# Kernel tuning notes

Measured on AMD Instinct MI355X. Metric: run time of the kernel, lower is better.

Reference implementation:

```python
import jax, jax.numpy as jnp
import numpy as np

B, N, E = 2, 32768, 32768
DIM = 3
MP_STEPS = 2
H = 32  # hidden width; original bug: depth == hidden width (range(hidden))


def _ln(x, g, b):
    m = jnp.mean(x, axis=-1, keepdims=True)
    v = jnp.var(x, axis=-1, keepdims=True)
    return (x - m) * jax.lax.rsqrt(v + 1e-5) * g + b


def _mlp(x, Win, bin_, Wh, bh, Wout, bout, lng=None, lnb=None):
    # Linear -> ReLU -> [LN] -> H x (Linear -> ReLU -> [LN]) -> Linear -> ReLU
    h = jax.nn.relu(x @ Win + bin_)
    if lng is not None:
        h = _ln(h, lng[0], lnb[0])
        def body(h, p):
            W, b_, g_, bb = p
            return _ln(jax.nn.relu(h @ W + b_), g_, bb), None
        h, _ = jax.lax.scan(body, h, (Wh, bh, lng[1:], lnb[1:]))
    else:
        def body(h, p):
            W, b_ = p
            return jax.nn.relu(h @ W + b_), None
        h, _ = jax.lax.scan(body, h, (Wh, bh))
    return jax.nn.relu(h @ Wout + bout)


def _mk(key, din, h, dout, ln, pref):
    ks = jax.random.split(key, 3)
    d = {
        pref + 'Win': jax.random.normal(ks[0], (din, h), jnp.float32) / np.sqrt(din).astype(np.float32),
        pref + 'bin': jnp.zeros((h,), jnp.float32),
        pref + 'Wh': jax.random.normal(ks[1], (h, h, h), jnp.float32) / np.sqrt(h).astype(np.float32),
        pref + 'bh': jnp.zeros((h, h), jnp.float32),
        pref + 'Wout': jax.random.normal(ks[2], (h, dout), jnp.float32) / np.sqrt(h).astype(np.float32),
        pref + 'bout': jnp.zeros((dout,), jnp.float32),
    }
    if ln:
        d[pref + 'lng'] = jnp.ones((h + 1, h), jnp.float32)
        d[pref + 'lnb'] = jnp.zeros((h + 1, h), jnp.float32)
    return d


def setup_inputs() -> dict:
    key = jax.random.key(0)
    ks = jax.random.split(key, 10)
    inp = {
        'nodes': jax.random.normal(ks[0], (B, N, 6), jnp.float32),
        'edges': jax.random.normal(ks[1], (B, E, 1), jnp.float32),
        'gvec': jax.random.normal(ks[2], (B,), jnp.float32),
        'senders': jax.random.randint(ks[3], (B, E), 0, N, jnp.int32),
        'receivers': jax.random.randint(ks[4], (B, E), 0, N, jnp.int32),
    }
    inp.update(_mk(ks[5], 6 + 1, H, 16, False, 'ne_'))          # node encoder: node_dim+global
    inp.update(_mk(ks[6], 1 + DIM + 1, H, 16, False, 'ed_'))    # edge encoder: edge_dim+dim+1
    inp.update(_mk(ks[7], 16 + 2 * 16 + 1, H, 16, True, 'pe_')) # edge processor
    inp.update(_mk(ks[8], 16 + 16 + 1, H, 16, True, 'pv_'))     # node processor
    inp.update(_mk(ks[9], 16, H, DIM, False, 'de_'))            # decoder
    return inp


def reference(nodes, edges, gvec, senders, receivers,
              ne_Win, ne_bin, ne_Wh, ne_bh, ne_Wout, ne_bout,
              ed_Win, ed_bin, ed_Wh, ed_bh, ed_Wout, ed_bout,
              pe_Win, pe_bin, pe_Wh, pe_bh, pe_Wout, pe_bout, pe_lng, pe_lnb,
              pv_Win, pv_bin, pv_Wh, pv_bh, pv_Wout, pv_bout, pv_lng, pv_lnb,
              de_Win, de_bin, de_Wh, de_bh, de_Wout, de_bout):
    g_node = jnp.broadcast_to(gvec[:, None, None], (B, N, 1))  # global repeated per node
    g_edge = jnp.broadcast_to(gvec[:, None, None], (B, E, 1))  # global repeated per edge
    x = jnp.concatenate([nodes, g_node], axis=-1)  # [B,N,7]

    # relative edge features from sender/receiver positions (first DIM cols)
    pos = x[..., :DIM]
    si = senders[:, :, None]
    ri = receivers[:, :, None]
    rel = jnp.take_along_axis(pos, si, axis=1) - jnp.take_along_axis(pos, ri, axis=1)  # [B,E,3]
    nrm = jnp.linalg.norm(rel, axis=-1, keepdims=True)
    e_in = jnp.concatenate([edges, rel, nrm], axis=-1)  # [B,E,5]

    ve = _mlp(x, ne_Win, ne_bin, ne_Wh, ne_bh, ne_Wout, ne_bout)       # [B,N,16]
    ee = _mlp(e_in, ed_Win, ed_bin, ed_Wh, ed_bh, ed_Wout, ed_bout)    # [B,E,16]

    seg = jax.vmap(lambda e, r: jax.ops.segment_sum(e, r, num_segments=N))

    for _ in range(MP_STEPS):
        # phi_e: gather sender/receiver node states, concat, edge MLP
        vs = jnp.take_along_axis(ve, si, axis=1)  # [B,E,16]
        vr = jnp.take_along_axis(ve, ri, axis=1)
        ee = _mlp(jnp.concatenate([ee, vs, vr, g_edge], axis=-1),
                  pe_Win, pe_bin, pe_Wh, pe_bh, pe_Wout, pe_bout, pe_lng, pe_lnb)
        # phi_v: scatter-add edge states into receiver nodes, concat, node MLP
        agg = seg(ee, receivers)  # [B,N,16]
        ve = _mlp(jnp.concatenate([agg, ve, g_node], axis=-1),
                  pv_Win, pv_bin, pv_Wh, pv_bh, pv_Wout, pv_bout, pv_lng, pv_lnb)

    return _mlp(ve, de_Win, de_bin, de_Wh, de_bh, de_Wout, de_bout)  # [B,N,3]
```

## Files before the change

### kernel.cpp

```cpp
#include <hip/hip_runtime.h>

#define BB 2
#define NN 32768
#define EN 32768

typedef unsigned int u32;
typedef __attribute__((ext_vector_type(8)))  short bf16x8;
typedef __attribute__((ext_vector_type(2)))  float f32x2;
typedef __attribute__((ext_vector_type(16))) float f32x16;

union U4 { uint4 u; bf16x8 h; };

__device__ __forceinline__ u32 pk2(float lo, float hi) {
    u32 r;
    asm("v_cvt_pk_bf16_f32 %0, %1, %2" : "=v"(r) : "v"(lo), "v"(hi));
    return r;
}

__device__ __forceinline__ float xor32_sum(float x) {
    float y = x;
    asm("v_permlane32_swap_b32 %0, %1" : "+v"(x), "+v"(y));
    return x + y;
}

__device__ __forceinline__ f32x16 MF32(bf16x8 a, bf16x8 b, f32x16 c) {
    return __builtin_amdgcn_mfma_f32_32x32x16_bf16(a, b, c, 0, 0, 0);
}

template<bool LN>
__device__ __forceinline__ void transform32(f32x16 D, bf16x8& B0, bf16x8& B1)
{
    f32x2 p0 = {D[0],D[1]},  p1 = {D[2],D[3]},  p2 = {D[4],D[5]},  p3 = {D[6],D[7]};
    f32x2 p4 = {D[8],D[9]},  p5 = {D[10],D[11]},p6 = {D[12],D[13]},p7 = {D[14],D[15]};
    const f32x2 zz = {0.f, 0.f};
    p0 = __builtin_elementwise_max(p0, zz); p1 = __builtin_elementwise_max(p1, zz);
    p2 = __builtin_elementwise_max(p2, zz); p3 = __builtin_elementwise_max(p3, zz);
    p4 = __builtin_elementwise_max(p4, zz); p5 = __builtin_elementwise_max(p5, zz);
    p6 = __builtin_elementwise_max(p6, zz); p7 = __builtin_elementwise_max(p7, zz);
    if (LN) {
        f32x2 sv = ((p0+p1)+(p2+p3)) + ((p4+p5)+(p6+p7));
        f32x2 ta = __builtin_elementwise_fma(p0,p0,
                   __builtin_elementwise_fma(p1,p1,
                   __builtin_elementwise_fma(p2,p2, p3*p3)));
        f32x2 tb = __builtin_elementwise_fma(p4,p4,
                   __builtin_elementwise_fma(p5,p5,
                   __builtin_elementwise_fma(p6,p6, p7*p7)));
        f32x2 tv = ta + tb;
        float s = xor32_sum(sv.x + sv.y);
        float t = xor32_sum(tv.x + tv.y);
        float mu  = s * (1.f/32.f);
        float var = fmaf(-mu, mu, t * (1.f/32.f));
        float rs  = rsqrtf(var + 1e-5f);
        float nt  = -mu * rs;
        f32x2 rs2 = {rs, rs}, nt2 = {nt, nt};
        p0 = __builtin_elementwise_fma(p0, rs2, nt2);
        p1 = __builtin_elementwise_fma(p1, rs2, nt2);
        p2 = __builtin_elementwise_fma(p2, rs2, nt2);
        p3 = __builtin_elementwise_fma(p3, rs2, nt2);
        p4 = __builtin_elementwise_fma(p4, rs2, nt2);
        p5 = __builtin_elementwise_fma(p5, rs2, nt2);
        p6 = __builtin_elementwise_fma(p6, rs2, nt2);
        p7 = __builtin_elementwise_fma(p7, rs2, nt2);
    }
    U4 c;
    c.u.x = pk2(p0.x,p0.y); c.u.y = pk2(p1.x,p1.y);
    c.u.z = pk2(p2.x,p2.y); c.u.w = pk2(p3.x,p3.y);
    B0 = c.h;
    c.u.x = pk2(p4.x,p4.y); c.u.y = pk2(p5.x,p5.y);
    c.u.z = pk2(p6.x,p6.y); c.u.w = pk2(p7.x,p7.y);
    B1 = c.h;
}

__device__ __forceinline__ f32x16 load_biasC(const float* WB, int base, int h) {
    const float4* p = (const float4*)(WB + base + h*16);
    float4 a = p[0], b = p[1], c = p[2], d = p[3];
    f32x16 C = {a.x,a.y,a.z,a.w, b.x,b.y,b.z,b.w,
                c.x,c.y,c.z,c.w, d.x,d.y,d.z,d.w};
    return C;
}

template<int NT, bool LN>
__device__ __forceinline__ f32x16 mlp32(const bf16x8* bIn,
    const u32* WL, const float* WB, int lane, int h)
{
    constexpr int HB = NT*256;
    constexpr int BO = HB + 16384;
    U4 c;
    f32x16 D = load_biasC(WB, 0, h);
    #pragma unroll
    for (int t = 0; t < NT; ++t) {
        c.u = *(const uint4*)(WL + t*256 + lane*4);
        D = MF32(c.h, bIn[t], D);
    }
    c.u = *(const uint4*)(WL + HB + lane*4);        bf16x8 w0 = c.h;
    c.u = *(const uint4*)(WL + HB + 256 + lane*4);  bf16x8 w1 = c.h;
    c.u = *(const uint4*)(WL + HB + 512 + lane*4);  bf16x8 x0 = c.h;
    c.u = *(const uint4*)(WL + HB + 768 + lane*4);  bf16x8 x1 = c.h;
    f32x16 pb = load_biasC(WB, 32, h);
    bf16x8 B0, B1;
    transform32<LN>(D, B0, B1);
    #pragma unroll 4
    for (int l = 0; l < 32; ++l) {
        const int lp = (l+2 < 32) ? l+2 : 31;
        c.u = *(const uint4*)(WL + HB + lp*512 + lane*4);       bf16x8 nw0 = c.h;
        c.u = *(const uint4*)(WL + HB + lp*512 + 256 + lane*4); bf16x8 nw1 = c.h;
        const int lb_ = (l+1 < 32) ? l+1 : 31;
        f32x16 nb = load_biasC(WB, 32 + lb_*32, h);
        f32x16 E = MF32(w0, B0, pb);
        E = MF32(w1, B1, E);
        transform32<LN>(E, B0, B1);
        w0 = x0; w1 = x1; x0 = nw0; x1 = nw1; pb = nb;
    }
    c.u = *(const uint4*)(WL + BO + lane*4);        bf16x8 o0 = c.h;
    c.u = *(const uint4*)(WL + BO + 256 + lane*4);  bf16x8 o1 = c.h;
    f32x16 Co = load_biasC(WB, 1056, h);
    f32x16 O = MF32(o0, B0, Co);
    O = MF32(o1, B1, O);
    return O;
}

__device__ __forceinline__ void stage_weights32(
    u32* WL, float* WB, const u32* __restrict__ Wp,
    const float* __restrict__ bin, const float* __restrict__ bhid,
    const float* __restrict__ bo, int wtot, int nbo, int tid, int nthr)
{
    const int lane  = tid & 63;
    const int base0 = (tid >> 6) * 256;
    const int step  = (nthr >> 6) * 256;
    for (int C = base0; C < wtot; C += step)
        __builtin_amdgcn_global_load_lds(
            (const __attribute__((address_space(1))) u32*)(Wp + C + lane*4),
            (__attribute__((address_space(3))) u32*)(WL + C), 16, 0, 0);
    for (int i = tid; i < 1088; i += nthr) {
        float v;
        if (i < 32) {
            int w = i, hh = w>>4, r = w&15;
            int f = (r&3) + 8*(r>>2) + 4*hh;
            v = bin[f];
        } else if (i < 1056) {
            int l = (i-32)>>5, w = (i-32)&31, hh = w>>4, r = w&15;
            int f = (r&3) + 8*(r>>2) + 4*hh;
            v = bhid[l*32 + f];
        } else {
            int w = i-1056, hh = w>>4, r = w&15;
            int f = (r&3) + 8*(r>>2) + 4*hh;
            v = (f < nbo) ? bo[f] : 0.f;
        }
        WB[i] = v;
    }
    __syncthreads();
}

__device__ __forceinline__ void pack_body32(
    const float* __restrict__ Win, const float* __restrict__ Wh,
    const float* __restrict__ Wout, const float* __restrict__ lng,
    u32* __restrict__ dst, int din, int dout, int NT, int lb, int tid)
{
    int t = lb * 256 + tid;
    int binW = NT * 256;
    int tot = binW + 16384 + 512;
    if (t >= tot) return;
    float lo, hi;
    if (t < binW) {
        int tt = t>>8, rem = t&255, ln_ = rem>>2, d = rem&3;
        int hh = ln_>>5, m = ln_&31;
        int f0 = 16*tt + 4*hh + 2*(d&1) + 8*(d>>1);
        lo = (f0   < din) ? Win[f0*32 + m]     : 0.f;
        hi = (f0+1 < din) ? Win[(f0+1)*32 + m] : 0.f;
    } else if (t < binW + 16384) {
        int u = t - binW, l = u>>9, v = u&511;
        int tt = v>>8, rem = v&255, ln_ = rem>>2, d = rem&3;
        int hh = ln_>>5, m = ln_&31;
        int f0 = 16*tt + 4*hh + 2*(d&1) + 8*(d>>1);
        lo = Wh[l*1024 + f0*32 + m];
        hi = Wh[l*1024 + (f0+1)*32 + m];
        if (lng) { lo *= lng[l*32 + f0]; hi *= lng[l*32 + f0 + 1]; }
    } else {
        int u = t - binW - 16384;
        int tt = u>>8, rem = u&255, ln_ = rem>>2, d = rem&3;
        int hh = ln_>>5, m = ln_&31;
        int f0 = 16*tt + 4*hh + 2*(d&1) + 8*(d>>1);
        lo = (m < dout) ? Wout[f0*dout + m]     : 0.f;
        hi = (m < dout) ? Wout[(f0+1)*dout + m] : 0.f;
        if (lng) { lo *= lng[1024 + f0]; hi *= lng[1024 + f0 + 1]; }
    }
    dst[t] = pk2(lo, hi);
}

__device__ __forceinline__ void fold_body(
    const float* __restrict__ Wh,   const float* __restrict__ bh,
    const float* __restrict__ Wout, const float* __restrict__ bout,
    const float* __restrict__ lnb,  float* __restrict__ fb, int lb, int tid)
{
    int j = lb * 256 + tid;
    if (j < 1024) {
        int l = j >> 5, jj = j & 31;
        float acc = bh[j];
        #pragma unroll
        for (int k = 0; k < 32; ++k)
            acc = fmaf(lnb[l*32 + k], Wh[l*1024 + k*32 + jj], acc);
        fb[j] = acc;
    } else if (j < 1024 + 16) {
        int jj = j - 1024;
        float acc = bout[jj];
        #pragma unroll
        for (int k = 0; k < 32; ++k)
            acc = fmaf(lnb[1024 + k], Wout[k*16 + jj], acc);
        fb[j] = acc;
    }
}

__global__ __launch_bounds__(256) void prep_kernel(
    const float* ne_Win, const float* ne_Wh, const float* ne_Wout,
    const float* ed_Win, const float* ed_Wh, const float* ed_Wout,
    const float* pe_Win, const float* pe_Wh, const float* pe_Wout,
    const float* pe_lng, const float* pe_lnb, const float* pe_bh, const float* pe_bout,
    const float* pv_Win, const float* pv_Wh, const float* pv_Wout,
    const float* pv_lng, const float* pv_lnb, const float* pv_bh, const float* pv_bout,
    const float* de_Win, const float* de_Wh, const float* de_Wout,
    u32* Wne, u32* Wed, u32* Wpe, u32* Wpv, u32* Wde,
    float* Fpe, float* Fpv)
{
    int bx = blockIdx.x, tid = threadIdx.x;
    if      (bx < 67)  pack_body32(ne_Win, ne_Wh, ne_Wout, nullptr, Wne,  7, 16, 1, bx,       tid);
    else if (bx < 134) pack_body32(ed_Win, ed_Wh, ed_Wout, nullptr, Wed,  5, 16, 1, bx - 67,  tid);
    else if (bx < 204) pack_body32(pe_Win, pe_Wh, pe_Wout, pe_lng,  Wpe, 49, 16, 4, bx - 134, tid);
    else if (bx < 273) pack_body32(pv_Win, pv_Wh, pv_Wout, pv_lng,  Wpv, 33, 16, 3, bx - 204, tid);
    else if (bx < 340) pack_body32(de_Win, de_Wh, de_Wout, nullptr, Wde, 16,  3, 1, bx - 273, tid);
    else if (bx < 345) fold_body(pe_Wh, pe_bh, pe_Wout, pe_bout, pe_lnb, Fpe, bx - 340, tid);
    else               fold_body(pv_Wh, pv_bh, pv_Wout, pv_bout, pv_lnb, Fpv, bx - 345, tid);
}

__device__ __forceinline__ bf16x8 stage_chunk(const float* __restrict__ arr,
                                              size_t e, int h)
{
    const int off = h*4;
    float4 a = *(const float4*)(arr + e*16 + off);
    float4 b = *(const float4*)(arr + e*16 + off + 8);
    U4 c;
    c.u.x = pk2(a.x, a.y); c.u.y = pk2(a.z, a.w);
    c.u.z = pk2(b.x, b.y); c.u.w = pk2(b.z, b.w);
    return c.h;
}

#define WAVE_SETUP \
    const int lane = threadIdx.x & 63; \
    const int wid  = threadIdx.x >> 6; \
    const int el = lane & 31, h = lane >> 5;

__global__ __launch_bounds__(512, 4) void encode_kernel(
    const float* __restrict__ nodes, const float* __restrict__ edges,
    const float* __restrict__ gvec,
    const int* __restrict__ senders, const int* __restrict__ receivers,
    const u32* __restrict__ Wne, const float* __restrict__ ne_bin,
    const float* __restrict__ ne_bh, const float* __restrict__ ne_bout,
    const u32* __restrict__ Wed, const float* __restrict__ ed_bin,
    const float* __restrict__ ed_bh, const float* __restrict__ ed_bout,
    float* __restrict__ ve, float* __restrict__ ee)
{
    __shared__ __align__(16) u32 SL[17152 + 1088];
    u32* WL = SL;
    float* WB = (float*)(SL + 17152);
    WAVE_SETUP
    const bool edge_stage = blockIdx.x >= 256;
    stage_weights32(WL, WB,
                    edge_stage ? Wed : Wne,
                    edge_stage ? ed_bin : ne_bin,
                    edge_stage ? ed_bh : ne_bh,
                    edge_stage ? ed_bout : ne_bout,
                    17152, 16, threadIdx.x, 512);
    const int lb = edge_stage ? (blockIdx.x - 256) : blockIdx.x;
    const int e = (lb*8 + wid)*32 + el;
    const int b = e >> 15;
    bf16x8 a0;
    {
        uint4 w; w.x = 0u; w.y = 0u; w.z = 0u; w.w = 0u;
        if (!edge_stage) {
            if (h == 0) {
                float2 v01 = *(const float2*)(nodes + (size_t)e*6);
                float2 v23 = *(const float2*)(nodes + (size_t)e*6 + 2);
                w.x = pk2(v01.x, v01.y); w.y = pk2(v23.x, v23.y);
            } else {
                float2 v45 = *(const float2*)(nodes + (size_t)e*6 + 4);
                w.x = pk2(v45.x, v45.y); w.y = pk2(gvec[b], 0.f);
            }
        } else {
            int s = senders[e], r = receivers[e];
            const float* ps = nodes + ((size_t)b*NN + s)*6;
            const float* pr = nodes + ((size_t)b*NN + r)*6;
            float2 s01 = *(const float2*)ps; float s2v = ps[2];
            float2 r01 = *(const float2*)pr; float r2v = pr[2];
            float r0 = s01.x - r01.x, r1 = s01.y - r01.y, r2 = s2v - r2v;
            if (h == 0) {
                w.x = pk2(edges[e], r0); w.y = pk2(r1, r2);
            } else {
                w.x = pk2(sqrtf(r0*r0 + r1*r1 + r2*r2), 0.f);
            }
        }
        U4 c; c.u = w; a0 = c.h;
    }
    float* dst = edge_stage ? ee : ve;
    f32x16 O = mlp32<1, false>(&a0, WL, WB, lane, h);
    float4 s1, s2;
    s1.x = fmaxf(O[0], 0.f); s1.y = fmaxf(O[1], 0.f);
    s1.z = fmaxf(O[2], 0.f); s1.w = fmaxf(O[3], 0.f);
    s2.x = fmaxf(O[4], 0.f); s2.y = fmaxf(O[5], 0.f);
    s2.z = fmaxf(O[6], 0.f); s2.w = fmaxf(O[7], 0.f);
    *(float4*)(dst + (size_t)e*16 + h*4)     = s1;
    *(float4*)(dst + (size_t)e*16 + h*4 + 8) = s2;
}

__global__ __launch_bounds__(512, 2) void edge_update_kernel(
    const float* __restrict__ gvec,
    const int* __restrict__ senders, const int* __restrict__ receivers,
    const float* __restrict__ ve, float* __restrict__ ee, float* __restrict__ agg,
    const u32* __restrict__ Wp, const float* __restrict__ bin,
    const float* __restrict__ fb)
{
    __shared__ __align__(16) u32 SL[17920 + 1088 + 8*544];
    u32* WL = SL;
    float* WB = (float*)(SL + 17920);
    WAVE_SETUP
    float* X = (float*)(SL + 19008) + wid*544;
    stage_weights32(WL, WB, Wp, bin, fb, fb + 1024, 17920, 16, threadIdx.x, 512);
    const int e0 = (blockIdx.x*8 + wid)*32;
    const int e  = e0 + el;
    const int b  = e >> 15;
    const int s  = senders[e], r_ = receivers[e];
    bf16x8 a[4];
    a[0] = stage_chunk(ee, (size_t)e, h);
    a[1] = stage_chunk(ve, (size_t)b*NN + s, h);
    a[2] = stage_chunk(ve, (size_t)b*NN + r_, h);
    {
        uint4 w; w.x = (h == 0) ? pk2(gvec[b], 0.f) : 0u;
        w.y = 0u; w.z = 0u; w.w = 0u;
        U4 c; c.u = w; a[3] = c.h;
    }
    f32x16 O = mlp32<4, true>(a, WL, WB, lane, h);
    float4 s1, s2;
    s1.x = fmaxf(O[0], 0.f); s1.y = fmaxf(O[1], 0.f);
    s1.z = fmaxf(O[2], 0.f); s1.w = fmaxf(O[3], 0.f);
    s2.x = fmaxf(O[4], 0.f); s2.y = fmaxf(O[5], 0.f);
    s2.z = fmaxf(O[6], 0.f); s2.w = fmaxf(O[7], 0.f);
    *(float4*)(ee + (size_t)e*16 + h*4)     = s1;
    *(float4*)(ee + (size_t)e*16 + h*4 + 8) = s2;
    *(float4*)(X + el*17 + h*4)     = s1;
    *(float4*)(X + el*17 + h*4 + 8) = s2;
    const int feat = lane & 15;
    #pragma unroll
    for (int rr = 0; rr < 8; ++rr) {
        int m = (lane >> 4)*8 + rr;
        float v = X[m*17 + feat];
        int rc = __shfl(r_, m);
        int eg = e0 + m;
        atomicAdd(agg + ((size_t)(eg >> 15)*NN + rc)*16 + feat, v);
    }
}

template<bool DEC>
__global__ __launch_bounds__(512, 2) void node_update_kernel(
    const float* __restrict__ gvec,
    const float* __restrict__ agg, float* __restrict__ ve,
    const u32* __restrict__ Wp, const float* __restrict__ bin,
    const float* __restrict__ fb,
    const u32* __restrict__ Wde, const float* __restrict__ de_bin,
    const float* __restrict__ de_bh, const float* __restrict__ de_bout,
    float* __restrict__ out)
{
    __shared__ __align__(16) u32 SL[DEC ? (18752 + 17152 + 1088) : 18752];
    u32* WL = SL;
    float* WB = (float*)(SL + 17664);
    u32* WL2 = SL + 18752;
    float* WB2 = (float*)(SL + 18752 + 17152);
    WAVE_SETUP
    stage_weights32(WL, WB, Wp, bin, fb, fb + 1024, 17664, 16, threadIdx.x, 512);
    if (DEC)
        stage_weights32(WL2, WB2, Wde, de_bin, de_bh, de_bout, 17152, 3, threadIdx.x, 512);
    const int e = (blockIdx.x*8 + wid)*32 + el;
    const int b = e >> 15;
    bf16x8 a[3];
    a[0] = stage_chunk(agg, (size_t)e, h);
    a[1] = stage_chunk(ve,  (size_t)e, h);
    {
        uint4 w; w.x = (h == 0) ? pk2(gvec[b], 0.f) : 0u;
        w.y = 0u; w.z = 0u; w.w = 0u;
        U4 c; c.u = w; a[2] = c.h;
    }
    f32x16 O = mlp32<3, true>(a, WL, WB, lane, h);
    if (!DEC) {
        float4 s1, s2;
        s1.x = fmaxf(O[0], 0.f); s1.y = fmaxf(O[1], 0.f);
        s1.z = fmaxf(O[2], 0.f); s1.w = fmaxf(O[3], 0.f);
        s2.x = fmaxf(O[4], 0.f); s2.y = fmaxf(O[5], 0.f);
        s2.z = fmaxf(O[6], 0.f); s2.w = fmaxf(O[7], 0.f);
        *(float4*)(ve + (size_t)e*16 + h*4)     = s1;
        *(float4*)(ve + (size_t)e*16 + h*4 + 8) = s2;
    } else {
        bf16x8 D0, D1;
        transform32<false>(O, D0, D1);
        f32x16 O2 = mlp32<1, false>(&D0, WL2, WB2, lane, h);
        if (h == 0) {
            out[(size_t)e*3 + 0] = fmaxf(O2[0], 0.f);
            out[(size_t)e*3 + 1] = fmaxf(O2[1], 0.f);
            out[(size_t)e*3 + 2] = fmaxf(O2[2], 0.f);
        }
    }
}

extern "C" void kernel_launch(void* const* d_in, const int* in_sizes, int n_in,
                              void* d_out, int out_size, void* d_ws, size_t ws_size,
                              hipStream_t stream)
{
    const float* nodes     = (const float*)d_in[0];
    const float* edges     = (const float*)d_in[1];
    const float* gvec      = (const float*)d_in[2];
    const int*   senders   = (const int*)  d_in[3];
    const int*   receivers = (const int*)  d_in[4];

    const float* ne_Win  = (const float*)d_in[5];
    const float* ne_bin  = (const float*)d_in[6];
    const float* ne_Wh   = (const float*)d_in[7];
    const float* ne_bh   = (const float*)d_in[8];
    const float* ne_Wout = (const float*)d_in[9];
    const float* ne_bout = (const float*)d_in[10];

    const float* ed_Win  = (const float*)d_in[11];
    const float* ed_bin  = (const float*)d_in[12];
    const float* ed_Wh   = (const float*)d_in[13];
    const float* ed_bh   = (const float*)d_in[14];
    const float* ed_Wout = (const float*)d_in[15];
    const float* ed_bout = (const float*)d_in[16];

    const float* pe_Win  = (const float*)d_in[17];
    const float* pe_bin  = (const float*)d_in[18];
    const float* pe_Wh   = (const float*)d_in[19];
    const float* pe_bh   = (const float*)d_in[20];
    const float* pe_Wout = (const float*)d_in[21];
    const float* pe_bout = (const float*)d_in[22];
    const float* pe_lng  = (const float*)d_in[23];
    const float* pe_lnb  = (const float*)d_in[24];

    const float* pv_Win  = (const float*)d_in[25];
    const float* pv_bin  = (const float*)d_in[26];
    const float* pv_Wh   = (const float*)d_in[27];
    const float* pv_bh   = (const float*)d_in[28];
    const float* pv_Wout = (const float*)d_in[29];
    const float* pv_bout = (const float*)d_in[30];
    const float* pv_lng  = (const float*)d_in[31];
    const float* pv_lnb  = (const float*)d_in[32];

    const float* de_Win  = (const float*)d_in[33];
    const float* de_bin  = (const float*)d_in[34];
    const float* de_Wh   = (const float*)d_in[35];
    const float* de_bh   = (const float*)d_in[36];
    const float* de_Wout = (const float*)d_in[37];
    const float* de_bout = (const float*)d_in[38];

    float* ve   = (float*)d_ws;
    float* ee   = ve   + (size_t)1048576;
    float* agg0 = ee   + (size_t)1048576;
    float* agg1 = agg0 + (size_t)1048576;
    u32* Wne = (u32*)(agg1 + (size_t)1048576);
    u32* Wed = Wne + 17152;
    u32* Wpe = Wed + 17152;
    u32* Wpv = Wpe + 17920;
    u32* Wde = Wpv + 17664;
    float* Fpe = (float*)(Wde + 17152);
    float* Fpv = Fpe + 1040;

    prep_kernel<<<350, dim3(256), 0, stream>>>(
        ne_Win, ne_Wh, ne_Wout,
        ed_Win, ed_Wh, ed_Wout,
        pe_Win, pe_Wh, pe_Wout, pe_lng, pe_lnb, pe_bh, pe_bout,
        pv_Win, pv_Wh, pv_Wout, pv_lng, pv_lnb, pv_bh, pv_bout,
        de_Win, de_Wh, de_Wout,
        Wne, Wed, Wpe, Wpv, Wde, Fpe, Fpv);

    hipMemsetAsync(agg0, 0, (size_t)2 * 1048576 * sizeof(float), stream);

    encode_kernel<<<512, dim3(512), 0, stream>>>(nodes, edges, gvec, senders, receivers,
        Wne, ne_bin, ne_bh, ne_bout,
        Wed, ed_bin, ed_bh, ed_bout, ve, ee);

    edge_update_kernel<<<256, dim3(512), 0, stream>>>(gvec, senders, receivers,
        ve, ee, agg0, Wpe, pe_bin, Fpe);
    node_update_kernel<false><<<256, dim3(512), 0, stream>>>(gvec, agg0, ve,
        Wpv, pv_bin, Fpv, Wde, de_bin, de_bh, de_bout, (float*)d_out);
    edge_update_kernel<<<256, dim3(512), 0, stream>>>(gvec, senders, receivers,
        ve, ee, agg1, Wpe, pe_bin, Fpe);
    node_update_kernel<true><<<256, dim3(512), 0, stream>>>(gvec, agg1, ve,
        Wpv, pv_bin, Fpv, Wde, de_bin, de_bh, de_bout, (float*)d_out);
}
```

Baseline: 241.6 us.

## Switch MLP chain from 32x32x16 to 16x16x32 MFMA with 16 rows per wave

Rewrites the per-wave MLP to process 16 rows with two 16x16x32 bf16 MFMAs per layer instead of one 32-row tile with two 32x32x16 MFMAs. The weight packing is re-laid out to match, and the input K-chunks are packed tighter (2 chunks instead of 3-4). Biases are read directly from global memory rather than staged in LDS. LDS use drops enough to raise occupancy bounds to 4, and grids double to keep the same coverage. The decoder reuses the LDS buffer after a sync instead of a second staging area. This trades the per-row work of the serial 32-layer dependency chain for more blocks and shorter MFMA latency. The risk is more weight reloads per row and uncached global bias loads.

```diff
diff --git a/kernel.cpp b/kernel.cpp
--- a/kernel.cpp
+++ b/kernel.cpp
@@ -7,7 +7,7 @@
 typedef unsigned int u32;
 typedef __attribute__((ext_vector_type(8)))  short bf16x8;
 typedef __attribute__((ext_vector_type(2)))  float f32x2;
-typedef __attribute__((ext_vector_type(16))) float f32x16;
+typedef __attribute__((ext_vector_type(4)))  float f32x4;
 
 union U4 { uint4 u; bf16x8 h; };
 
@@ -17,169 +17,136 @@
     return r;
 }
 
-__device__ __forceinline__ float xor32_sum(float x) {
-    float y = x;
-    asm("v_permlane32_swap_b32 %0, %1" : "+v"(x), "+v"(y));
-    return x + y;
-}
-
-__device__ __forceinline__ f32x16 MF32(bf16x8 a, bf16x8 b, f32x16 c) {
-    return __builtin_amdgcn_mfma_f32_32x32x16_bf16(a, b, c, 0, 0, 0);
+__device__ __forceinline__ float red4(float v) {
+    int x = __builtin_amdgcn_ds_swizzle(__builtin_bit_cast(int, v), 0x401F);
+    v += __builtin_bit_cast(float, x);
+    float w = v;
+    asm("v_permlane32_swap_b32 %0, %1" : "+v"(v), "+v"(w));
+    return v + w;
+}
+
+__device__ __forceinline__ f32x4 MF16(bf16x8 a, bf16x8 b, f32x4 c) {
+    return __builtin_amdgcn_mfma_f32_16x16x32_bf16(a, b, c, 0, 0, 0);
 }
 
 template<bool LN>
-__device__ __forceinline__ void transform32(f32x16 D, bf16x8& B0, bf16x8& B1)
-{
-    f32x2 p0 = {D[0],D[1]},  p1 = {D[2],D[3]},  p2 = {D[4],D[5]},  p3 = {D[6],D[7]};
-    f32x2 p4 = {D[8],D[9]},  p5 = {D[10],D[11]},p6 = {D[12],D[13]},p7 = {D[14],D[15]};
+__device__ __forceinline__ bf16x8 transform16(f32x4 lo, f32x4 hi)
+{
+    f32x2 q0 = {lo[0],lo[1]}, q1 = {lo[2],lo[3]};
+    f32x2 q2 = {hi[0],hi[1]}, q3 = {hi[2],hi[3]};
     const f32x2 zz = {0.f, 0.f};
-    p0 = __builtin_elementwise_max(p0, zz); p1 = __builtin_elementwise_max(p1, zz);
-    p2 = __builtin_elementwise_max(p2, zz); p3 = __builtin_elementwise_max(p3, zz);
-    p4 = __builtin_elementwise_max(p4, zz); p5 = __builtin_elementwise_max(p5, zz);
-    p6 = __builtin_elementwise_max(p6, zz); p7 = __builtin_elementwise_max(p7, zz);
+    q0 = __builtin_elementwise_max(q0, zz); q1 = __builtin_elementwise_max(q1, zz);
+    q2 = __builtin_elementwise_max(q2, zz); q3 = __builtin_elementwise_max(q3, zz);
     if (LN) {
-        f32x2 sv = ((p0+p1)+(p2+p3)) + ((p4+p5)+(p6+p7));
-        f32x2 ta = __builtin_elementwise_fma(p0,p0,
-                   __builtin_elementwise_fma(p1,p1,
-                   __builtin_elementwise_fma(p2,p2, p3*p3)));
-        f32x2 tb = __builtin_elementwise_fma(p4,p4,
-                   __builtin_elementwise_fma(p5,p5,
-                   __builtin_elementwise_fma(p6,p6, p7*p7)));
-        f32x2 tv = ta + tb;
-        float s = xor32_sum(sv.x + sv.y);
-        float t = xor32_sum(tv.x + tv.y);
+        f32x2 sv = (q0+q1)+(q2+q3);
+        f32x2 tv = __builtin_elementwise_fma(q0,q0,
+                   __builtin_elementwise_fma(q1,q1,
+                   __builtin_elementwise_fma(q2,q2, q3*q3)));
+        float s = red4(sv.x + sv.y);
+        float t = red4(tv.x + tv.y);
         float mu  = s * (1.f/32.f);
         float var = fmaf(-mu, mu, t * (1.f/32.f));
         float rs  = rsqrtf(var + 1e-5f);
         float nt  = -mu * rs;
         f32x2 rs2 = {rs, rs}, nt2 = {nt, nt};
-        p0 = __builtin_elementwise_fma(p0, rs2, nt2);
-        p1 = __builtin_elementwise_fma(p1, rs2, nt2);
-        p2 = __builtin_elementwise_fma(p2, rs2, nt2);
-        p3 = __builtin_elementwise_fma(p3, rs2, nt2);
-        p4 = __builtin_elementwise_fma(p4, rs2, nt2);
-        p5 = __builtin_elementwise_fma(p5, rs2, nt2);
-        p6 = __builtin_elementwise_fma(p6, rs2, nt2);
-        p7 = __builtin_elementwise_fma(p7, rs2, nt2);
+        q0 = __builtin_elementwise_fma(q0, rs2, nt2);
+        q1 = __builtin_elementwise_fma(q1, rs2, nt2);
+        q2 = __builtin_elementwise_fma(q2, rs2, nt2);
+        q3 = __builtin_elementwise_fma(q3, rs2, nt2);
     }
     U4 c;
-    c.u.x = pk2(p0.x,p0.y); c.u.y = pk2(p1.x,p1.y);
-    c.u.z = pk2(p2.x,p2.y); c.u.w = pk2(p3.x,p3.y);
-    B0 = c.h;
-    c.u.x = pk2(p4.x,p4.y); c.u.y = pk2(p5.x,p5.y);
-    c.u.z = pk2(p6.x,p6.y); c.u.w = pk2(p7.x,p7.y);
-    B1 = c.h;
-}
-
-__device__ __forceinline__ f32x16 load_biasC(const float* WB, int base, int h) {
-    const float4* p = (const float4*)(WB + base + h*16);
-    float4 a = p[0], b = p[1], c = p[2], d = p[3];
-    f32x16 C = {a.x,a.y,a.z,a.w, b.x,b.y,b.z,b.w,
-                c.x,c.y,c.z,c.w, d.x,d.y,d.z,d.w};
-    return C;
-}
-
-template<int NT, bool LN>
-__device__ __forceinline__ f32x16 mlp32(const bf16x8* bIn,
-    const u32* WL, const float* WB, int lane, int h)
-{
-    constexpr int HB = NT*256;
+    c.u.x = pk2(q0.x,q0.y); c.u.y = pk2(q1.x,q1.y);
+    c.u.z = pk2(q2.x,q2.y); c.u.w = pk2(q3.x,q3.y);
+    return c.h;
+}
+
+template<int NT, bool LN, bool OUT3>
+__device__ __forceinline__ f32x4 mlp16(const bf16x8* bIn, const u32* WL,
+    const float* __restrict__ bin, const float* __restrict__ bh,
+    const float* __restrict__ bo, int lane, int g)
+{
+    constexpr int HB = NT*512;
     constexpr int BO = HB + 16384;
     U4 c;
-    f32x16 D = load_biasC(WB, 0, h);
+    f32x4 Dlo = *(const f32x4*)(bin + 4*g);
+    f32x4 Dhi = *(const f32x4*)(bin + 16 + 4*g);
     #pragma unroll
     for (int t = 0; t < NT; ++t) {
-        c.u = *(const uint4*)(WL + t*256 + lane*4);
-        D = MF32(c.h, bIn[t], D);
-    }
-    c.u = *(const uint4*)(WL + HB + lane*4);        bf16x8 w0 = c.h;
-    c.u = *(const uint4*)(WL + HB + 256 + lane*4);  bf16x8 w1 = c.h;
-    c.u = *(const uint4*)(WL + HB + 512 + lane*4);  bf16x8 x0 = c.h;
-    c.u = *(const uint4*)(WL + HB + 768 + lane*4);  bf16x8 x1 = c.h;
-    f32x16 pb = load_biasC(WB, 32, h);
-    bf16x8 B0, B1;
-    transform32<LN>(D, B0, B1);
+        c.u = *(const uint4*)(WL + (2*t)*256 + lane*4);
+        Dlo = MF16(c.h, bIn[t], Dlo);
+        c.u = *(const uint4*)(WL + (2*t+1)*256 + lane*4);
+        Dhi = MF16(c.h, bIn[t], Dhi);
+    }
+    c.u = *(const uint4*)(WL + HB + lane*4);        bf16x8 wl0 = c.h;
+    c.u = *(const uint4*)(WL + HB + 256 + lane*4);  bf16x8 wh0 = c.h;
+    c.u = *(const uint4*)(WL + HB + 512 + lane*4);  bf16x8 wl1 = c.h;
+    c.u = *(const uint4*)(WL + HB + 768 + lane*4);  bf16x8 wh1 = c.h;
+    f32x4 cbl = *(const f32x4*)(bh + 4*g);
+    f32x4 cbh = *(const f32x4*)(bh + 16 + 4*g);
+    bf16x8 Bf = transform16<LN>(Dlo, Dhi);
     #pragma unroll 4
     for (int l = 0; l < 32; ++l) {
         const int lp = (l+2 < 32) ? l+2 : 31;
-        c.u = *(const uint4*)(WL + HB + lp*512 + lane*4);       bf16x8 nw0 = c.h;
-        c.u = *(const uint4*)(WL + HB + lp*512 + 256 + lane*4); bf16x8 nw1 = c.h;
+        c.u = *(const uint4*)(WL + HB + lp*512 + lane*4);       bf16x8 nwl = c.h;
+        c.u = *(const uint4*)(WL + HB + lp*512 + 256 + lane*4); bf16x8 nwh = c.h;
         const int lb_ = (l+1 < 32) ? l+1 : 31;
-        f32x16 nb = load_biasC(WB, 32 + lb_*32, h);
-        f32x16 E = MF32(w0, B0, pb);
-        E = MF32(w1, B1, E);
-        transform32<LN>(E, B0, B1);
-        w0 = x0; w1 = x1; x0 = nw0; x1 = nw1; pb = nb;
-    }
-    c.u = *(const uint4*)(WL + BO + lane*4);        bf16x8 o0 = c.h;
-    c.u = *(const uint4*)(WL + BO + 256 + lane*4);  bf16x8 o1 = c.h;
-    f32x16 Co = load_biasC(WB, 1056, h);
-    f32x16 O = MF32(o0, B0, Co);
-    O = MF32(o1, B1, O);
-    return O;
-}
-
-__device__ __forceinline__ void stage_weights32(
-    u32* WL, float* WB, const u32* __restrict__ Wp,
-    const float* __restrict__ bin, const float* __restrict__ bhid,
-    const float* __restrict__ bo, int wtot, int nbo, int tid, int nthr)
-{
-    const int lane  = tid & 63;
-    const int base0 = (tid >> 6) * 256;
-    const int step  = (nthr >> 6) * 256;
-    for (int C = base0; C < wtot; C += step)
+        f32x4 nbl = *(const f32x4*)(bh + lb_*32 + 4*g);
+        f32x4 nbh = *(const f32x4*)(bh + lb_*32 + 16 + 4*g);
+        f32x4 Elo = MF16(wl0, Bf, cbl);
+        f32x4 Ehi = MF16(wh0, Bf, cbh);
+        Bf = transform16<LN>(Elo, Ehi);
+        wl0 = wl1; wh0 = wh1; wl1 = nwl; wh1 = nwh; cbl = nbl; cbh = nbh;
+    }
+    c.u = *(const uint4*)(WL + BO + lane*4);
+    f32x4 Co;
+    if (OUT3) {
+        Co = (f32x4){0.f, 0.f, 0.f, 0.f};
+        if (g == 0) { Co[0] = bo[0]; Co[1] = bo[1]; Co[2] = bo[2]; }
+    } else {
+        Co = *(const f32x4*)(bo + 4*g);
+    }
+    return MF16(c.h, Bf, Co);
+}
+
+__device__ __forceinline__ void stage_w(u32* WL, const u32* __restrict__ Wp,
+                                        int wtot, int tid)
+{
+    const int lane = tid & 63;
+    for (int C = (tid >> 6)*256; C < wtot; C += 8*256)
         __builtin_amdgcn_global_load_lds(
             (const __attribute__((address_space(1))) u32*)(Wp + C + lane*4),
             (__attribute__((address_space(3))) u32*)(WL + C), 16, 0, 0);
-    for (int i = tid; i < 1088; i += nthr) {
-        float v;
-        if (i < 32) {
-            int w = i, hh = w>>4, r = w&15;
-            int f = (r&3) + 8*(r>>2) + 4*hh;
-            v = bin[f];
-        } else if (i < 1056) {
-            int l = (i-32)>>5, w = (i-32)&31, hh = w>>4, r = w&15;
-            int f = (r&3) + 8*(r>>2) + 4*hh;
-            v = bhid[l*32 + f];
-        } else {
-            int w = i-1056, hh = w>>4, r = w&15;
-            int f = (r&3) + 8*(r>>2) + 4*hh;
-            v = (f < nbo) ? bo[f] : 0.f;
-        }
-        WB[i] = v;
-    }
     __syncthreads();
 }
 
-__device__ __forceinline__ void pack_body32(
+__device__ __forceinline__ void pack_body16(
     const float* __restrict__ Win, const float* __restrict__ Wh,
     const float* __restrict__ Wout, const float* __restrict__ lng,
     u32* __restrict__ dst, int din, int dout, int NT, int lb, int tid)
 {
     int t = lb * 256 + tid;
-    int binW = NT * 256;
-    int tot = binW + 16384 + 512;
+    int binW = NT * 512;
+    int tot = binW + 16384 + 256;
     if (t >= tot) return;
     float lo, hi;
     if (t < binW) {
-        int tt = t>>8, rem = t&255, ln_ = rem>>2, d = rem&3;
-        int hh = ln_>>5, m = ln_&31;
-        int f0 = 16*tt + 4*hh + 2*(d&1) + 8*(d>>1);
+        int tt = t>>9, v = t&511, H = v>>8, rem = v&255, ln_ = rem>>2, d = rem&3;
+        int g = ln_>>4, m = (ln_&15) + H*16;
+        int f0 = 32*tt + 16*(d>>1) + 4*g + 2*(d&1);
         lo = (f0   < din) ? Win[f0*32 + m]     : 0.f;
         hi = (f0+1 < din) ? Win[(f0+1)*32 + m] : 0.f;
     } else if (t < binW + 16384) {
-        int u = t - binW, l = u>>9, v = u&511;
-        int tt = v>>8, rem = v&255, ln_ = rem>>2, d = rem&3;
-        int hh = ln_>>5, m = ln_&31;
-        int f0 = 16*tt + 4*hh + 2*(d&1) + 8*(d>>1);
+        int u = t - binW, l = u>>9, v = u&511, H = v>>8, rem = v&255;
+        int ln_ = rem>>2, d = rem&3;
+        int g = ln_>>4, m = (ln_&15) + H*16;
+        int f0 = 16*(d>>1) + 4*g + 2*(d&1);
         lo = Wh[l*1024 + f0*32 + m];
         hi = Wh[l*1024 + (f0+1)*32 + m];
         if (lng) { lo *= lng[l*32 + f0]; hi *= lng[l*32 + f0 + 1]; }
     } else {
-        int u = t - binW - 16384;
-        int tt = u>>8, rem = u&255, ln_ = rem>>2, d = rem&3;
-        int hh = ln_>>5, m = ln_&31;
-        int f0 = 16*tt + 4*hh + 2*(d&1) + 8*(d>>1);
+        int u = t - binW - 16384, ln_ = u>>2, d = u&3;
+        int g = ln_>>4, m = ln_&15;
+        int f0 = 16*(d>>1) + 4*g + 2*(d&1);
         lo = (m < dout) ? Wout[f0*dout + m]     : 0.f;
         hi = (m < dout) ? Wout[(f0+1)*dout + m] : 0.f;
         if (lng) { lo *= lng[1024 + f0]; hi *= lng[1024 + f0 + 1]; }
@@ -222,31 +189,19 @@
     float* Fpe, float* Fpv)
 {
     int bx = blockIdx.x, tid = threadIdx.x;
-    if      (bx < 67)  pack_body32(ne_Win, ne_Wh, ne_Wout, nullptr, Wne,  7, 16, 1, bx,       tid);
-    else if (bx < 134) pack_body32(ed_Win, ed_Wh, ed_Wout, nullptr, Wed,  5, 16, 1, bx - 67,  tid);
-    else if (bx < 204) pack_body32(pe_Win, pe_Wh, pe_Wout, pe_lng,  Wpe, 49, 16, 4, bx - 134, tid);
-    else if (bx < 273) pack_body32(pv_Win, pv_Wh, pv_Wout, pv_lng,  Wpv, 33, 16, 3, bx - 204, tid);
-    else if (bx < 340) pack_body32(de_Win, de_Wh, de_Wout, nullptr, Wde, 16,  3, 1, bx - 273, tid);
-    else if (bx < 345) fold_body(pe_Wh, pe_bh, pe_Wout, pe_bout, pe_lnb, Fpe, bx - 340, tid);
-    else               fold_body(pv_Wh, pv_bh, pv_Wout, pv_bout, pv_lnb, Fpv, bx - 345, tid);
-}
-
-__device__ __forceinline__ bf16x8 stage_chunk(const float* __restrict__ arr,
-                                              size_t e, int h)
-{
-    const int off = h*4;
-    float4 a = *(const float4*)(arr + e*16 + off);
-    float4 b = *(const float4*)(arr + e*16 + off + 8);
-    U4 c;
-    c.u.x = pk2(a.x, a.y); c.u.y = pk2(a.z, a.w);
-    c.u.z = pk2(b.x, b.y); c.u.w = pk2(b.z, b.w);
-    return c.h;
+    if      (bx < 67)  pack_body16(ne_Win, ne_Wh, ne_Wout, nullptr, Wne,  7, 16, 1, bx,       tid);
+    else if (bx < 134) pack_body16(ed_Win, ed_Wh, ed_Wout, nullptr, Wed,  5, 16, 1, bx - 67,  tid);
+    else if (bx < 203) pack_body16(pe_Win, pe_Wh, pe_Wout, pe_lng,  Wpe, 49, 16, 2, bx - 134, tid);
+    else if (bx < 272) pack_body16(pv_Win, pv_Wh, pv_Wout, pv_lng,  Wpv, 33, 16, 2, bx - 203, tid);
+    else if (bx < 339) pack_body16(de_Win, de_Wh, de_Wout, nullptr, Wde, 16,  3, 1, bx - 272, tid);
+    else if (bx < 344) fold_body(pe_Wh, pe_bh, pe_Wout, pe_bout, pe_lnb, Fpe, bx - 339, tid);
+    else               fold_body(pv_Wh, pv_bh, pv_Wout, pv_bout, pv_lnb, Fpv, bx - 344, tid);
 }
 
 #define WAVE_SETUP \
     const int lane = threadIdx.x & 63; \
     const int wid  = threadIdx.x >> 6; \
-    const int el = lane & 31, h = lane >> 5;
+    const int el = lane & 15, g = lane >> 4;
 
 __global__ __launch_bounds__(512, 4) void encode_kernel(
     const float* __restrict__ nodes, const float* __restrict__ edges,
@@ -258,107 +213,98 @@
     const float* __restrict__ ed_bh, const float* __restrict__ ed_bout,
     float* __restrict__ ve, float* __restrict__ ee)
 {
-    __shared__ __align__(16) u32 SL[17152 + 1088];
-    u32* WL = SL;
-    float* WB = (float*)(SL + 17152);
+    __shared__ __align__(16) u32 SL[17152];
     WAVE_SETUP
-    const bool edge_stage = blockIdx.x >= 256;
-    stage_weights32(WL, WB,
-                    edge_stage ? Wed : Wne,
-                    edge_stage ? ed_bin : ne_bin,
-                    edge_stage ? ed_bh : ne_bh,
-                    edge_stage ? ed_bout : ne_bout,
-                    17152, 16, threadIdx.x, 512);
-    const int lb = edge_stage ? (blockIdx.x - 256) : blockIdx.x;
-    const int e = (lb*8 + wid)*32 + el;
+    const bool es = blockIdx.x >= 512;
+    stage_w(SL, es ? Wed : Wne, 17152, threadIdx.x);
+    const int lb = es ? (blockIdx.x - 512) : blockIdx.x;
+    const int e = (lb*8 + wid)*16 + el;
     const int b = e >> 15;
     bf16x8 a0;
     {
         uint4 w; w.x = 0u; w.y = 0u; w.z = 0u; w.w = 0u;
-        if (!edge_stage) {
-            if (h == 0) {
+        if (!es) {
+            if (g == 0) {
                 float2 v01 = *(const float2*)(nodes + (size_t)e*6);
                 float2 v23 = *(const float2*)(nodes + (size_t)e*6 + 2);
                 w.x = pk2(v01.x, v01.y); w.y = pk2(v23.x, v23.y);
-            } else {
+            } else if (g == 1) {
                 float2 v45 = *(const float2*)(nodes + (size_t)e*6 + 4);
                 w.x = pk2(v45.x, v45.y); w.y = pk2(gvec[b], 0.f);
             }
         } else {
-            int s = senders[e], r = receivers[e];
-            const float* ps = nodes + ((size_t)b*NN + s)*6;
-            const float* pr = nodes + ((size_t)b*NN + r)*6;
-            float2 s01 = *(const float2*)ps; float s2v = ps[2];
-            float2 r01 = *(const float2*)pr; float r2v = pr[2];
-            float r0 = s01.x - r01.x, r1 = s01.y - r01.y, r2 = s2v - r2v;
-            if (h == 0) {
-                w.x = pk2(edges[e], r0); w.y = pk2(r1, r2);
-            } else {
-                w.x = pk2(sqrtf(r0*r0 + r1*r1 + r2*r2), 0.f);
+            if (g < 2) {
+                int s = senders[e], r = receivers[e];
+                const float* ps = nodes + ((size_t)b*NN + s)*6;
+                const float* pr = nodes + ((size_t)b*NN + r)*6;
+                float2 s01 = *(const float2*)ps; float s2v = ps[2];
+                float2 r01 = *(const float2*)pr; float r2v = pr[2];
+                float r0 = s01.x - r01.x, r1 = s01.y - r01.y, r2 = s2v - r2v;
+                if (g == 0) {
+                    w.x = pk2(edges[e], r0); w.y = pk2(r1, r2);
+                } else {
+                    w.x = pk2(sqrtf(r0*r0 + r1*r1 + r2*r2), 0.f);
+                }
             }
         }
         U4 c; c.u = w; a0 = c.h;
     }
-    float* dst = edge_stage ? ee : ve;
-    f32x16 O = mlp32<1, false>(&a0, WL, WB, lane, h);
-    float4 s1, s2;
+    f32x4 O = mlp16<1, false, false>(&a0, SL,
+                es ? ed_bin : ne_bin, es ? ed_bh : ne_bh,
+                es ? ed_bout : ne_bout, lane, g);
+    float4 s1;
     s1.x = fmaxf(O[0], 0.f); s1.y = fmaxf(O[1], 0.f);
     s1.z = fmaxf(O[2], 0.f); s1.w = fmaxf(O[3], 0.f);
-    s2.x = fmaxf(O[4], 0.f); s2.y = fmaxf(O[5], 0.f);
-    s2.z = fmaxf(O[6], 0.f); s2.w = fmaxf(O[7], 0.f);
-    *(float4*)(dst + (size_t)e*16 + h*4)     = s1;
-    *(float4*)(dst + (size_t)e*16 + h*4 + 8) = s2;
-}
-
-__global__ __launch_bounds__(512, 2) void edge_update_kernel(
+    *(float4*)((es ? ee : ve) + (size_t)e*16 + 4*g) = s1;
+}
+
+__global__ __launch_bounds__(512, 4) void edge_update_kernel(
     const float* __restrict__ gvec,
     const int* __restrict__ senders, const int* __restrict__ receivers,
     const float* __restrict__ ve, float* __restrict__ ee, float* __restrict__ agg,
     const u32* __restrict__ Wp, const float* __restrict__ bin,
     const float* __restrict__ fb)
 {
-    __shared__ __align__(16) u32 SL[17920 + 1088 + 8*544];
+    __shared__ __align__(16) u32 SL[17664 + 8*272];
     u32* WL = SL;
-    float* WB = (float*)(SL + 17920);
     WAVE_SETUP
-    float* X = (float*)(SL + 19008) + wid*544;
-    stage_weights32(WL, WB, Wp, bin, fb, fb + 1024, 17920, 16, threadIdx.x, 512);
-    const int e0 = (blockIdx.x*8 + wid)*32;
+    float* X = (float*)(SL + 17664) + wid*272;
+    stage_w(WL, Wp, 17664, threadIdx.x);
+    const int e0 = (blockIdx.x*8 + wid)*16;
     const int e  = e0 + el;
     const int b  = e >> 15;
     const int s  = senders[e], r_ = receivers[e];
-    bf16x8 a[4];
-    a[0] = stage_chunk(ee, (size_t)e, h);
-    a[1] = stage_chunk(ve, (size_t)b*NN + s, h);
-    a[2] = stage_chunk(ve, (size_t)b*NN + r_, h);
+    float4 fee = *(const float4*)(ee + (size_t)e*16 + 4*g);
+    float4 fvs = *(const float4*)(ve + ((size_t)b*NN + s )*16 + 4*g);
+    float4 fvr = *(const float4*)(ve + ((size_t)b*NN + r_)*16 + 4*g);
+    bf16x8 a[2];
     {
-        uint4 w; w.x = (h == 0) ? pk2(gvec[b], 0.f) : 0u;
-        w.y = 0u; w.z = 0u; w.w = 0u;
-        U4 c; c.u = w; a[3] = c.h;
-    }
-    f32x16 O = mlp32<4, true>(a, WL, WB, lane, h);
-    float4 s1, s2;
+        uint4 w;
+        w.x = pk2(fee.x, fee.y); w.y = pk2(fee.z, fee.w);
+        w.z = pk2(fvs.x, fvs.y); w.w = pk2(fvs.z, fvs.w);
+        U4 c; c.u = w; a[0] = c.h;
+        w.x = pk2(fvr.x, fvr.y); w.y = pk2(fvr.z, fvr.w);
+        w.z = (g == 0) ? pk2(gvec[b], 0.f) : 0u; w.w = 0u;
+        c.u = w; a[1] = c.h;
+    }
+    f32x4 O = mlp16<2, true, false>(a, WL, bin, fb, fb + 1024, lane, g);
+    float4 s1;
     s1.x = fmaxf(O[0], 0.f); s1.y = fmaxf(O[1], 0.f);
     s1.z = fmaxf(O[2], 0.f); s1.w = fmaxf(O[3], 0.f);
-    s2.x = fmaxf(O[4], 0.f); s2.y = fmaxf(O[5], 0.f);
-    s2.z = fmaxf(O[6], 0.f); s2.w = fmaxf(O[7], 0.f);
-    *(float4*)(ee + (size_t)e*16 + h*4)     = s1;
-    *(float4*)(ee + (size_t)e*16 + h*4 + 8) = s2;
-    *(float4*)(X + el*17 + h*4)     = s1;
-    *(float4*)(X + el*17 + h*4 + 8) = s2;
+    *(float4*)(ee + (size_t)e*16 + 4*g) = s1;
+    *(float4*)(X + el*17 + 4*g) = s1;
     const int feat = lane & 15;
     #pragma unroll
-    for (int rr = 0; rr < 8; ++rr) {
-        int m = (lane >> 4)*8 + rr;
+    for (int rr = 0; rr < 4; ++rr) {
+        int m = (lane >> 4) + rr*4;
         float v = X[m*17 + feat];
         int rc = __shfl(r_, m);
-        int eg = e0 + m;
-        atomicAdd(agg + ((size_t)(eg >> 15)*NN + rc)*16 + feat, v);
+        atomicAdd(agg + ((size_t)b*NN + rc)*16 + feat, v);
     }
 }
 
 template<bool DEC>
-__global__ __launch_bounds__(512, 2) void node_update_kernel(
+__global__ __launch_bounds__(512, 4) void node_update_kernel(
     const float* __restrict__ gvec,
     const float* __restrict__ agg, float* __restrict__ ve,
     const u32* __restrict__ Wp, const float* __restrict__ bin,
@@ -367,39 +313,43 @@
     const float* __restrict__ de_bh, const float* __restrict__ de_bout,
     float* __restrict__ out)
 {
-    __shared__ __align__(16) u32 SL[DEC ? (18752 + 17152 + 1088) : 18752];
-    u32* WL = SL;
-    float* WB = (float*)(SL + 17664);
-    u32* WL2 = SL + 18752;
-    float* WB2 = (float*)(SL + 18752 + 17152);
+    __shared__ __align__(16) u32 SL[17664];
     WAVE_SETUP
-    stage_weights32(WL, WB, Wp, bin, fb, fb + 1024, 17664, 16, threadIdx.x, 512);
-    if (DEC)
-        stage_weights32(WL2, WB2, Wde, de_bin, de_bh, de_bout, 17152, 3, threadIdx.x, 512);
-    const int e = (blockIdx.x*8 + wid)*32 + el;
+    stage_w(SL, Wp, 17664, threadIdx.x);
+    const int e = (blockIdx.x*8 + wid)*16 + el;
     const int b = e >> 15;
-    bf16x8 a[3];
-    a[0] = stage_chunk(agg, (size_t)e, h);
-    a[1] = stage_chunk(ve,  (size_t)e, h);
+    float4 fa = *(const float4*)(agg + (size_t)e*16 + 4*g);
+    float4 fv = *(const float4*)(ve  + (size_t)e*16 + 4*g);
+    bf16x8 a[2];
     {
-        uint4 w; w.x = (h == 0) ? pk2(gvec[b], 0.f) : 0u;
+        uint4 w;
+        w.x = pk2(fa.x, fa.y); w.y = pk2(fa.z, fa.w);
+        w.z = pk2(fv.x, fv.y); w.w = pk2(fv.z, fv.w);
+        U4 c; c.u = w; a[0] = c.h;
+        w.x = (g == 0) ? pk2(gvec[b], 0.f) : 0u;
         w.y = 0u; w.z = 0u; w.w = 0u;
-        U4 c; c.u = w; a[2] = c.h;
-    }
-    f32x16 O = mlp32<3, true>(a, WL, WB, lane, h);
+        c.u = w; a[1] = c.h;
+    }
+    f32x4 O = mlp16<2, true, false>(a, SL, bin, fb, fb + 1024, lane, g);
     if (!DEC) {
-        float4 s1, s2;
+        float4 s1;
         s1.x = fmaxf(O[0], 0.f); s1.y = fmaxf(O[1], 0.f);
         s1.z = fmaxf(O[2], 0.f); s1.w = fmaxf(O[3], 0.f);
-        s2.x = fmaxf(O[4], 0.f); s2.y = fmaxf(O[5], 0.f);
-        s2.z = fmaxf(O[6], 0.f); s2.w = fmaxf(O[7], 0.f);
-        *(float4*)(ve + (size_t)e*16 + h*4)     = s1;
-        *(float4*)(ve + (size_t)e*16 + h*4 + 8) = s2;
+        *(float4*)(ve + (size_t)e*16 + 4*g) = s1;
     } else {
-        bf16x8 D0, D1;
-        transform32<false>(O, D0, D1);
-        f32x16 O2 = mlp32<1, false>(&D0, WL2, WB2, lane, h);
-        if (h == 0) {
+        __syncthreads();
+        stage_w(SL, Wde, 17152, threadIdx.x);
+        bf16x8 d0;
+        {
+            float o0 = fmaxf(O[0], 0.f), o1 = fmaxf(O[1], 0.f);
+            float o2 = fmaxf(O[2], 0.f), o3 = fmaxf(O[3], 0.f);
+            U4 c;
+            c.u.x = pk2(o0, o1); c.u.y = pk2(o2, o3);
+            c.u.z = 0u; c.u.w = 0u;
+            d0 = c.h;
+        }
+        f32x4 O2 = mlp16<1, false, true>(&d0, SL, de_bin, de_bh, de_bout, lane, g);
+        if (g == 0) {
             out[(size_t)e*3 + 0] = fmaxf(O2[0], 0.f);
             out[(size_t)e*3 + 1] = fmaxf(O2[1], 0.f);
             out[(size_t)e*3 + 2] = fmaxf(O2[2], 0.f);
@@ -463,12 +413,12 @@
     u32* Wne = (u32*)(agg1 + (size_t)1048576);
     u32* Wed = Wne + 17152;
     u32* Wpe = Wed + 17152;
-    u32* Wpv = Wpe + 17920;
+    u32* Wpv = Wpe + 17664;
     u32* Wde = Wpv + 17664;
     float* Fpe = (float*)(Wde + 17152);
     float* Fpv = Fpe + 1040;
 
-    prep_kernel<<<350, dim3(256), 0, stream>>>(
+    prep_kernel<<<349, dim3(256), 0, stream>>>(
         ne_Win, ne_Wh, ne_Wout,
         ed_Win, ed_Wh, ed_Wout,
         pe_Win, pe_Wh, pe_Wout, pe_lng, pe_lnb, pe_bh, pe_bout,
@@ -478,16 +428,16 @@
 
     hipMemsetAsync(agg0, 0, (size_t)2 * 1048576 * sizeof(float), stream);
 
-    encode_kernel<<<512, dim3(512), 0, stream>>>(nodes, edges, gvec, senders, receivers,
+    encode_kernel<<<1024, dim3(512), 0, stream>>>(nodes, edges, gvec, senders, receivers,
         Wne, ne_bin, ne_bh, ne_bout,
         Wed, ed_bin, ed_bh, ed_bout, ve, ee);
 
-    edge_update_kernel<<<256, dim3(512), 0, stream>>>(gvec, senders, receivers,
+    edge_update_kernel<<<512, dim3(512), 0, stream>>>(gvec, senders, receivers,
         ve, ee, agg0, Wpe, pe_bin, Fpe);
-    node_update_kernel<false><<<256, dim3(512), 0, stream>>>(gvec, agg0, ve,
+    node_update_kernel<false><<<512, dim3(512), 0, stream>>>(gvec, agg0, ve,
         Wpv, pv_bin, Fpv, Wde, de_bin, de_bh, de_bout, (float*)d_out);
-    edge_update_kernel<<<256, dim3(512), 0, stream>>>(gvec, senders, receivers,
+    edge_update_kernel<<<512, dim3(512), 0, stream>>>(gvec, senders, receivers,
         ve, ee, agg1, Wpe, pe_bin, Fpe);
-    node_update_kernel<true><<<256, dim3(512), 0, stream>>>(gvec, agg1, ve,
+    node_update_kernel<true><<<512, dim3(512), 0, stream>>>(gvec, agg1, ve,
         Wpv, pv_bin, Fpv, Wde, de_bin, de_bh, de_bout, (float*)d_out);
 }
```

New measurement: 255.6 us. +5.8%, slower.
